# Optimization experiments

Hardware: AMD Instinct MI355X
Metric: run time of the kernel (lower is better)

## Reference

```python
import jax, jax.numpy as jnp
import numpy as np

N = 50000      # nodes
E = 800000     # edges
IN = 128       # in_channels
HID = 32       # hidden_channels per head
HEADS = 4
OUT = 16       # out_channels
NEG_SLOPE_ATT = 0.2   # GATv2Conv default negative_slope
NEG_SLOPE_ACT = 0.01  # F.leaky_relu default
EPS = 1e-16


def setup_inputs() -> dict:
    key = jax.random.key(0)
    ks = jax.random.split(key, 13)
    d1 = HEADS * HID  # 128
    g = lambda k, shape, fan: jax.random.normal(k, shape, jnp.float32) * (1.0 / np.sqrt(fan))
    return {
        "x": jax.random.normal(ks[0], (N, IN), jnp.float32),
        "edge_index": jax.random.randint(ks[1], (2, E), 0, N, dtype=jnp.int32),
        "edge_weight": jax.random.uniform(ks[2], (E,), jnp.float32),
        # conv1 (GATv2): lin_l, lin_r, att, bias
        "Wl1": g(ks[3], (IN, d1), IN), "Wr1": g(ks[4], (IN, d1), IN),
        "att1": g(ks[5], (HEADS, HID), HID), "b1": jnp.zeros((d1,), jnp.float32),
        # conv2
        "Wl2": g(ks[6], (d1, d1), d1), "Wr2": g(ks[7], (d1, d1), d1),
        "att2": g(ks[8], (HEADS, HID), HID), "b2": jnp.zeros((d1,), jnp.float32),
        # classifier
        "Wc": g(ks[9], (d1, OUT), d1), "bc": jnp.zeros((OUT,), jnp.float32),
    }


def gatv2_layer(x, Wl, Wr, att, bias, src, dst):
    n = x.shape[0]
    xl = (x @ Wl).reshape(n, HEADS, HID)  # source transform
    xr = (x @ Wr).reshape(n, HEADS, HID)  # target transform
    m = xl[src] + xr[dst]                                    # [Etot, H, C]
    e = jnp.sum(jax.nn.leaky_relu(m, NEG_SLOPE_ATT) * att, axis=-1)  # [Etot, H]
    # segment softmax over incoming edges of each target node
    emax = jax.ops.segment_max(e, dst, num_segments=n)       # [N, H]
    ex = jnp.exp(e - emax[dst])
    denom = jax.ops.segment_sum(ex, dst, num_segments=n)     # [N, H]
    alpha = ex / (denom[dst] + EPS)                          # [Etot, H]
    out = jax.ops.segment_sum(xl[src] * alpha[:, :, None], dst, num_segments=n)  # [N, H, C]
    return out.reshape(n, HEADS * HID) + bias


def reference(x, edge_index, edge_weight, Wl1, Wr1, att1, b1, Wl2, Wr2, att2, b2, Wc, bc):
    # GATv2Conv default add_self_loops=True
    loops = jnp.arange(N, dtype=edge_index.dtype)
    src = jnp.concatenate([edge_index[0], loops])
    dst = jnp.concatenate([edge_index[1], loops])
    h = gatv2_layer(x, Wl1, Wr1, att1, b1, src, dst)
    h = jax.nn.leaky_relu(h, NEG_SLOPE_ACT)
    h = gatv2_layer(h, Wl2, Wr2, att2, b2, src, dst)
    h = jax.nn.leaky_relu(h, NEG_SLOPE_ACT)
    logits = h @ Wc + bc
    return (logits, h)
```

## Files before the change

kernel.cpp:

```cpp
#include <hip/hip_runtime.h>
#include <hip/hip_fp16.h>


#define LOG2E 1.4426950408889634f
#define AST 40

typedef short bf16x8 __attribute__((ext_vector_type(8)));
typedef float f32x4 __attribute__((ext_vector_type(4)));

__device__ __forceinline__ unsigned short f2bf(float f) {
  union { float f; unsigned u; } x; x.f = f;
  unsigned r = x.u + 0x7fffu + ((x.u >> 16) & 1u);
  return (unsigned short)(r >> 16);
}
__device__ __forceinline__ float bf2f(unsigned short h) {
  union { unsigned u; float f; } x; x.u = ((unsigned)h) << 16;
  return x.f;
}
__device__ __forceinline__ void split4(float4 v, ushort4& h, ushort4& l) {
  h.x = f2bf(v.x); l.x = f2bf(v.x - bf2f(h.x));
  h.y = f2bf(v.y); l.y = f2bf(v.y - bf2f(h.y));
  h.z = f2bf(v.z); l.z = f2bf(v.z - bf2f(h.z));
  h.w = f2bf(v.w); l.w = f2bf(v.w - bf2f(h.w));
}


__global__ __launch_bounds__(256) void zero_i32(int* __restrict__ p, int n) {
  int i = blockIdx.x * 256 + threadIdx.x;
  if (i < n) p[i] = 0;
}

__global__ __launch_bounds__(256) void scan_blk(const int* __restrict__ cnt,
                                                int* __restrict__ excl,
                                                int* __restrict__ bsum, int n) {
  __shared__ int s[256];
  int t = threadIdx.x, i = blockIdx.x * 256 + t;
  int v = (i < n) ? (cnt[i] + 1) : 0;
  s[t] = v;
  __syncthreads();
#pragma unroll
  for (int off = 1; off < 256; off <<= 1) {
    int u = (t >= off) ? s[t - off] : 0;
    __syncthreads();
    s[t] += u;
    __syncthreads();
  }
  if (i < n) excl[i] = s[t] - v;
  if (t == 255) bsum[blockIdx.x] = s[255];
}

__global__ __launch_bounds__(256) void scan_bsum(int* __restrict__ bsum, int nb,
                                                 int* __restrict__ row_start, int n) {
  __shared__ int s[256];
  int t = threadIdx.x;
  int v = (t < nb) ? bsum[t] : 0;
  s[t] = v;
  __syncthreads();
#pragma unroll
  for (int off = 1; off < 256; off <<= 1) {
    int u = (t >= off) ? s[t - off] : 0;
    __syncthreads();
    s[t] += u;
    __syncthreads();
  }
  if (t < nb) bsum[t] = s[t] - v;
  if (t == 255) row_start[n] = s[255];
}

__global__ __launch_bounds__(256) void scan_add(int* __restrict__ row_start,
                                                const int* __restrict__ bsum,
                                                int* __restrict__ wpos,
                                                int* __restrict__ csr,
                                                int n, int padBase) {
  int i = blockIdx.x * 256 + threadIdx.x;
  if (i < n) {
    int r = row_start[i] + bsum[blockIdx.x];
    row_start[i] = r;
    wpos[i] = r + 1;
    csr[r] = i;
  }
  if (blockIdx.x == 0 && threadIdx.x < 16) csr[padBase + threadIdx.x] = 0;
}

__global__ __launch_bounds__(256) void convert_count(
    const float* __restrict__ Wl1, const float* __restrict__ Wr1,
    const float* __restrict__ Wl2, const float* __restrict__ Wr2,
    unsigned short* __restrict__ BT1h, unsigned short* __restrict__ BT1l,
    unsigned short* __restrict__ BT2h, unsigned short* __restrict__ BT2l,
    const int* __restrict__ dst, int* __restrict__ cnt, int E) {
  int b = blockIdx.x;
  if (b >= 256) {
    int i = (b - 256) * 256 + threadIdx.x;
    if (i < E) atomicAdd(&cnt[dst[i]], 1);
    return;
  }
  const float* Wl = (b < 128) ? Wl1 : Wl2;
  const float* Wr = (b < 128) ? Wr1 : Wr2;
  unsigned short* BTh = (b < 128) ? BT1h : BT2h;
  unsigned short* BTl = (b < 128) ? BT1l : BT2l;
  int idx = (b & 127) * 256 + threadIdx.x;
  int col = idx >> 7, k = idx & 127;
  float v = (col < 128) ? Wl[k * 128 + col] : Wr[k * 128 + (col - 128)];
  unsigned short h = f2bf(v);
  BTh[idx] = h;
  BTl[idx] = f2bf(v - bf2f(h));
}

enum { IN_F32 = 0, IN_F16 = 1 };
#define NSCAT 1152
#define NCHUNK 128
template <int MODE, int FUSE>
__global__ __launch_bounds__(256) void gemm_mfma(
    const float* __restrict__ Af, const __half* __restrict__ Af16,
    const unsigned short* __restrict__ BTh, const unsigned short* __restrict__ BTl,
    __half* __restrict__ Cl, __half* __restrict__ Cr, int nrows,
    const int* __restrict__ esrc, const int* __restrict__ edst,
    int* __restrict__ wpos, int* __restrict__ csr, int E, int sliceSize) {
  __shared__ __align__(16) unsigned short smem[4 * 128 * AST];
  int tid = threadIdx.x;
  int bx, by;
  if (FUSE) {
    int g = blockIdx.x / 9, r = blockIdx.x - g * 9;
    if (r < 5) {
      int sid = g * 5 + r;
      if (sid < NSCAT) {
        int slice = blockIdx.x & 7;
        int chunk = (g >> 3) * 5;
        for (int gp = g & ~7; gp < g; ++gp)
          chunk += (((slice - gp) & 7) < 5) ? 1 : 0;
        if (chunk < NCHUNK) {
          int per = (E + NCHUNK - 1) / NCHUNK;
          int b0 = chunk * per;
          int ee = min(b0 + per, E);
          int lo = slice * sliceSize, hi = lo + sliceSize;
          int i = b0 + tid;
          for (; i + 768 < ee; i += 1024) {
            int d0 = edst[i];
            int d1 = edst[i + 256];
            int d2 = edst[i + 512];
            int d3 = edst[i + 768];
            if (d0 >= lo && d0 < hi) {
              int s = esrc[i];
              int p = atomicAdd(&wpos[d0], 1); csr[p] = s;
            }
            if (d1 >= lo && d1 < hi) {
              int s = esrc[i + 256];
              int p = atomicAdd(&wpos[d1], 1); csr[p] = s;
            }
            if (d2 >= lo && d2 < hi) {
              int s = esrc[i + 512];
              int p = atomicAdd(&wpos[d2], 1); csr[p] = s;
            }
            if (d3 >= lo && d3 < hi) {
              int s = esrc[i + 768];
              int p = atomicAdd(&wpos[d3], 1); csr[p] = s;
            }
          }
          for (; i < ee; i += 256) {
            int d = edst[i];
            if (d >= lo && d < hi) {
              int s = esrc[i];
              int p = atomicAdd(&wpos[d], 1); csr[p] = s;
            }
          }
        }
      }
      return;
    }
    int gid = g * 4 + (r - 5);
    int nbx = (nrows + 127) >> 7;
    if (gid >= nbx * 2) return;
    bx = gid >> 1;
    by = gid & 1;
  } else {
    bx = blockIdx.x;
    by = blockIdx.y;
  }

  unsigned short* sAh = smem;
  unsigned short* sAl = smem + 5120;
  unsigned short* sBh = smem + 10240;
  unsigned short* sBl = smem + 15360;

  int wave = tid >> 6, lane = tid & 63;
  int rowBase = bx * 128;
  int colBase = by * 128;
  int rowHalf = (wave >> 1) * 64;
  int colHalf = (wave & 1) * 64;
  int l15 = lane & 15, quad = lane >> 4;

  f32x4 acc[4][4];
#pragma unroll
  for (int m = 0; m < 4; ++m)
#pragma unroll
    for (int n = 0; n < 4; ++n) acc[m][n] = (f32x4){0.f, 0.f, 0.f, 0.f};

  for (int kc = 0; kc < 4; ++kc) {
#pragma unroll
    for (int i = 0; i < 2; ++i) {
      int idx = tid + i * 256;
      int row = idx >> 2, seg = idx & 3;
      int gr = rowBase + row;
      float4 v0 = make_float4(0.f, 0.f, 0.f, 0.f), v1 = v0;
      if (MODE == IN_F32) {
        if (gr < nrows) {
          v0 = *(const float4*)&Af[(size_t)gr * 128 + kc * 32 + seg * 8];
          v1 = *(const float4*)&Af[(size_t)gr * 128 + kc * 32 + seg * 8 + 4];
        }
      } else {
        if (gr < nrows) {
          uint4 raw = *(const uint4*)&Af16[(size_t)gr * 128 + kc * 32 + seg * 8];
          const __half* hp = (const __half*)&raw;
          v0 = make_float4(__half2float(hp[0]), __half2float(hp[1]),
                           __half2float(hp[2]), __half2float(hp[3]));
          v1 = make_float4(__half2float(hp[4]), __half2float(hp[5]),
                           __half2float(hp[6]), __half2float(hp[7]));
        }
      }
      ushort4 h0, l0, h1, l1;
      split4(v0, h0, l0);
      split4(v1, h1, l1);
      *(ushort4*)&sAh[row * AST + seg * 8] = h0;
      *(ushort4*)&sAh[row * AST + seg * 8 + 4] = h1;
      *(ushort4*)&sAl[row * AST + seg * 8] = l0;
      *(ushort4*)&sAl[row * AST + seg * 8 + 4] = l1;
    }
#pragma unroll
    for (int i = 0; i < 2; ++i) {
      int idx = tid + i * 256;
      int col = idx >> 2, seg = idx & 3;
      *(uint4*)&sBh[col * AST + seg * 8] =
          *(const uint4*)&BTh[(size_t)(colBase + col) * 128 + kc * 32 + seg * 8];
      *(uint4*)&sBl[col * AST + seg * 8] =
          *(const uint4*)&BTl[(size_t)(colBase + col) * 128 + kc * 32 + seg * 8];
    }
    __syncthreads();

    bf16x8 afh[4], afl[4], bfh[4], bfl[4];
#pragma unroll
    for (int m = 0; m < 4; ++m) {
      int r = rowHalf + m * 16 + l15;
      afh[m] = *(const bf16x8*)&sAh[r * AST + quad * 8];
      afl[m] = *(const bf16x8*)&sAl[r * AST + quad * 8];
    }
#pragma unroll
    for (int n = 0; n < 4; ++n) {
      int cc = colHalf + n * 16 + l15;
      bfh[n] = *(const bf16x8*)&sBh[cc * AST + quad * 8];
      bfl[n] = *(const bf16x8*)&sBl[cc * AST + quad * 8];
    }
    __builtin_amdgcn_s_setprio(1);
#pragma unroll
    for (int m = 0; m < 4; ++m)
#pragma unroll
      for (int n = 0; n < 4; ++n) {
        acc[m][n] = __builtin_amdgcn_mfma_f32_16x16x32_bf16(afh[m], bfh[n], acc[m][n], 0, 0, 0);
        acc[m][n] = __builtin_amdgcn_mfma_f32_16x16x32_bf16(afh[m], bfl[n], acc[m][n], 0, 0, 0);
        acc[m][n] = __builtin_amdgcn_mfma_f32_16x16x32_bf16(afl[m], bfh[n], acc[m][n], 0, 0, 0);
      }
    __builtin_amdgcn_s_setprio(0);
    __syncthreads();
  }

  __half* __restrict__ C = (by == 0) ? Cl : Cr;
#pragma unroll
  for (int m = 0; m < 4; ++m)
#pragma unroll
    for (int r = 0; r < 4; ++r) {
      int grow = rowBase + rowHalf + m * 16 + quad * 4 + r;
      if (grow < nrows) {
#pragma unroll
        for (int n = 0; n < 4; ++n)
          C[(size_t)grow * 128 + colHalf + n * 16 + l15] = __float2half(acc[m][n][r]);
      }
    }
}

__global__ __launch_bounds__(256) void gat_attn(const __half* __restrict__ xl,
                                                const __half* __restrict__ xr,
                                                const int* __restrict__ row_start,
                                                const int* __restrict__ csr,
                                                const float* __restrict__ att,
                                                const float* __restrict__ bias,
                                                float* __restrict__ ofp,
                                                __half* __restrict__ oh16,
                                                int n_nodes) {
  int node = blockIdx.x * 4 + (threadIdx.x >> 6);
  if (node >= n_nodes) return;
  int lane = threadIdx.x & 63;
  int slot = lane >> 4;
  int l15 = lane & 15;
  int c0 = l15 * 8;

  float fxr[8];
  {
    uint4 raw = *(const uint4*)&xr[(size_t)node * 128 + c0];
    const __half* hp = (const __half*)&raw;
#pragma unroll
    for (int k = 0; k < 8; ++k) fxr[k] = __half2float(hp[k]);
  }
  float a06[8], a04[8];
  {
    float4 a0 = *(const float4*)&att[c0];
    float4 a1 = *(const float4*)&att[c0 + 4];
    float av[8] = {a0.x, a0.y, a0.z, a0.w, a1.x, a1.y, a1.z, a1.w};
    const float C06 = 0.6f * LOG2E, C04 = 0.4f * LOG2E;
#pragma unroll
    for (int k = 0; k < 8; ++k) { a06[k] = av[k] * C06; a04[k] = av[k] * C04; }
  }

  float acc[8];
#pragma unroll
  for (int k = 0; k < 8; ++k) acc[k] = 0.f;
  float lsum = 0.f;

#define EDGE_BODY(SRC, PVALID)                                                 \
  {                                                                            \
    uint4 raw = *(const uint4*)&xl[(size_t)(unsigned)(SRC)*128 + c0];          \
    const __half* hp = (const __half*)&raw;                                    \
    float e = 0.f;                                                             \
    _Pragma("unroll") for (int k = 0; k < 8; ++k) {                            \
      float t = __half2float(hp[k]) + fxr[k];                                  \
      e = fmaf(a06[k], t, e);                                                  \
      e = fmaf(a04[k], fabsf(t), e);                                           \
    }                                                                          \
    e += __shfl_xor(e, 1);                                                     \
    e += __shfl_xor(e, 2);                                                     \
    float p = (PVALID) ? __builtin_amdgcn_exp2f(e) : 0.f;                      \
    lsum += p;                                                                 \
    _Pragma("unroll") for (int k = 0; k < 8; ++k)                              \
        acc[k] = fmaf(p, __half2float(hp[k]), acc[k]);                         \
  }

  int beg = row_start[node], end = row_start[node + 1];
  int deg = end - beg;
  int fullEnd = beg + (deg & ~15);

  for (int base = beg; base < fullEnd; base += 16) {
    int b0 = base + 4 * slot;
    int s0 = csr[b0], s1 = csr[b0 + 1], s2 = csr[b0 + 2], s3 = csr[b0 + 3];
    EDGE_BODY(s0, true);
    EDGE_BODY(s1, true);
    EDGE_BODY(s2, true);
    EDGE_BODY(s3, true);
  }
  for (int base = fullEnd; base < end; base += 4) {
    int idx = base + slot;
    int src = csr[idx];
    EDGE_BODY(src, idx < end);
  }
#undef EDGE_BODY

  lsum += __shfl_xor(lsum, 16);
  lsum += __shfl_xor(lsum, 32);
#pragma unroll
  for (int k = 0; k < 8; ++k) {
    acc[k] += __shfl_xor(acc[k], 16);
    acc[k] += __shfl_xor(acc[k], 32);
  }

  if (slot == 0) {
    float4 b0v = *(const float4*)&bias[c0];
    float4 b1v = *(const float4*)&bias[c0 + 4];
    float bv[8] = {b0v.x, b0v.y, b0v.z, b0v.w, b1v.x, b1v.y, b1v.z, b1v.w};
    float inv = 1.f / (lsum + 1e-16f);
    float o[8];
#pragma unroll
    for (int k = 0; k < 8; ++k) {
      float v = fmaf(acc[k], inv, bv[k]);
      o[k] = fmaf(0.495f, fabsf(v), 0.505f * v);
    }
    if (ofp) {
      *(float4*)&ofp[(size_t)node * 128 + c0] = make_float4(o[0], o[1], o[2], o[3]);
      *(float4*)&ofp[(size_t)node * 128 + c0 + 4] = make_float4(o[4], o[5], o[6], o[7]);
    }
    if (oh16) {
      ushort4 ha, hb;
      ha.x = __half_as_ushort(__float2half(o[0]));
      ha.y = __half_as_ushort(__float2half(o[1]));
      ha.z = __half_as_ushort(__float2half(o[2]));
      ha.w = __half_as_ushort(__float2half(o[3]));
      hb.x = __half_as_ushort(__float2half(o[4]));
      hb.y = __half_as_ushort(__float2half(o[5]));
      hb.z = __half_as_ushort(__float2half(o[6]));
      hb.w = __half_as_ushort(__float2half(o[7]));
      *(ushort4*)&oh16[(size_t)node * 128 + c0] = ha;
      *(ushort4*)&oh16[(size_t)node * 128 + c0 + 4] = hb;
    }
  }
}

__global__ __launch_bounds__(256) void classifier_kernel(const float4* __restrict__ h4,
                                                         const float* __restrict__ Wc,
                                                         const float* __restrict__ bc,
                                                         float* __restrict__ logits,
                                                         int n) {
  __shared__ float sW[2048];
  __shared__ float sb[16];
  int t = threadIdx.x;
#pragma unroll
  for (int i = 0; i < 8; ++i) sW[t + i * 256] = Wc[t + i * 256];
  if (t < 16) sb[t] = bc[t];
  __syncthreads();
  int node = blockIdx.x * 256 + t;
  if (node >= n) return;
  float acc[16];
#pragma unroll
  for (int o = 0; o < 16; ++o) acc[o] = sb[o];
  for (int c4 = 0; c4 < 32; ++c4) {
    float4 hv = h4[(unsigned)node * 32 + c4];
    const float* w = &sW[c4 * 64];
#pragma unroll
    for (int o = 0; o < 16; ++o) {
      acc[o] = fmaf(hv.x, w[o], acc[o]);
      acc[o] = fmaf(hv.y, w[16 + o], acc[o]);
      acc[o] = fmaf(hv.z, w[32 + o], acc[o]);
      acc[o] = fmaf(hv.w, w[48 + o], acc[o]);
    }
  }
#pragma unroll
  for (int q = 0; q < 4; ++q)
    *(float4*)&logits[(size_t)node * 16 + q * 4] =
        make_float4(acc[q * 4], acc[q * 4 + 1], acc[q * 4 + 2], acc[q * 4 + 3]);
}


extern "C" void kernel_launch(void* const* d_in, const int* in_sizes, int n_in,
                              void* d_out, int out_size, void* d_ws, size_t ws_size,
                              hipStream_t stream) {
  const float* x    = (const float*)d_in[0];
  const int*   ei   = (const int*)d_in[1];
  const float* Wl1  = (const float*)d_in[3];
  const float* Wr1  = (const float*)d_in[4];
  const float* att1 = (const float*)d_in[5];
  const float* b1   = (const float*)d_in[6];
  const float* Wl2  = (const float*)d_in[7];
  const float* Wr2  = (const float*)d_in[8];
  const float* att2 = (const float*)d_in[9];
  const float* b2   = (const float*)d_in[10];
  const float* Wc   = (const float*)d_in[11];
  const float* bc   = (const float*)d_in[12];

  const int N = in_sizes[0] / 128;
  const int E = in_sizes[1] / 2;

  float* outp   = (float*)d_out;
  float* logits = outp;
  float* hout   = outp + (size_t)N * 16;
  __half* h1f16 = (__half*)hout;

  char* ws = (char*)d_ws;
  __half* xlbuf = (__half*)ws;                ws += (size_t)N * 128 * 2;
  __half* xrbuf = (__half*)ws;                ws += (size_t)N * 128 * 2;
  unsigned short* WT1h = (unsigned short*)ws; ws += 256 * 128 * 2;
  unsigned short* WT1l = (unsigned short*)ws; ws += 256 * 128 * 2;
  unsigned short* WT2h = (unsigned short*)ws; ws += 256 * 128 * 2;
  unsigned short* WT2l = (unsigned short*)ws; ws += 256 * 128 * 2;
  int* cnt       = (int*)ws;                  ws += (size_t)N * 4;
  int* row_start = (int*)ws;                  ws += (size_t)(N + 1) * 4;
  int* wpos      = (int*)ws;                  ws += (size_t)N * 4;
  int* bsum      = (int*)ws;                  ws += 256 * 4;
  int* csr       = (int*)ws;                  ws += (size_t)(E + N + 16) * 4;

  const int* esrc = ei;
  const int* edst = ei + E;

  int gN = (N + 255) / 256, gE = (E + 255) / 256;
  int gAttn = (N + 3) / 4;
  int sliceSize = (N + 7) / 8;

  int nbx = (N + 127) / 128;
  int nGemm = nbx * 2;
  int groups = (NSCAT + 4) / 5;
  int g2 = (nGemm + 3) / 4;
  if (g2 > groups) groups = g2;
  int gFused = groups * 9;

  zero_i32<<<gN, 256, 0, stream>>>(cnt, N);
  convert_count<<<256 + gE, 256, 0, stream>>>(Wl1, Wr1, Wl2, Wr2,
                                              WT1h, WT1l, WT2h, WT2l,
                                              edst, cnt, E);
  scan_blk<<<gN, 256, 0, stream>>>(cnt, row_start, bsum, N);
  scan_bsum<<<1, 256, 0, stream>>>(bsum, gN, row_start, N);
  scan_add<<<gN, 256, 0, stream>>>(row_start, bsum, wpos, csr, N, E + N);

  gemm_mfma<IN_F32, 1><<<gFused, 256, 0, stream>>>(
      x, nullptr, WT1h, WT1l, xlbuf, xrbuf, N,
      esrc, edst, wpos, csr, E, sliceSize);
  gat_attn<<<gAttn, 256, 0, stream>>>(xlbuf, xrbuf, row_start, csr, att1, b1,
                                      nullptr, h1f16, N);

  gemm_mfma<IN_F16, 0><<<dim3(nbx, 2), 256, 0, stream>>>(
      nullptr, h1f16, WT2h, WT2l, xlbuf, xrbuf, N,
      nullptr, nullptr, nullptr, nullptr, 0, 0);
  gat_attn<<<gAttn, 256, 0, stream>>>(xlbuf, xrbuf, row_start, csr, att2, b2,
                                      hout, nullptr, N);

  classifier_kernel<<<(N + 255) / 256, 256, 0, stream>>>((const float4*)hout, Wc, bc,
                                                         logits, N);
}
```

Baseline: 314.3 us.

## Pre-bucket edges by destination slice during counting to avoid rescanning all edges

The counting kernel now also partitions edges into 8 destination-slice buckets of (src,dst) pairs, using shared-memory ranks and one global atomic per block per slice. The fused GEMM's scatter blocks then read only their slice's bucket instead of scanning every edge and filtering by range. This removes the roughly 8x redundant reads of the edge list in the scatter phase, at the cost of an extra bucket write pass and a fixed per-slice capacity that could overflow on skewed destination distributions. The separate zeroing kernel is replaced by a memset that also clears the bucket cursors.

```diff
diff --git a/kernel.cpp b/kernel.cpp
--- a/kernel.cpp
+++ b/kernel.cpp
@@ -24,11 +24,6 @@
   h.w = f2bf(v.w); l.w = f2bf(v.w - bf2f(h.w));
 }
 
-
-__global__ __launch_bounds__(256) void zero_i32(int* __restrict__ p, int n) {
-  int i = blockIdx.x * 256 + threadIdx.x;
-  if (i < n) p[i] = 0;
-}
 
 __global__ __launch_bounds__(256) void scan_blk(const int* __restrict__ cnt,
                                                 int* __restrict__ excl,
@@ -82,23 +77,54 @@
   if (blockIdx.x == 0 && threadIdx.x < 16) csr[padBase + threadIdx.x] = 0;
 }
 
+#define EPB 1024
 __global__ __launch_bounds__(256) void convert_count(
     const float* __restrict__ Wl1, const float* __restrict__ Wr1,
     const float* __restrict__ Wl2, const float* __restrict__ Wr2,
     unsigned short* __restrict__ BT1h, unsigned short* __restrict__ BT1l,
     unsigned short* __restrict__ BT2h, unsigned short* __restrict__ BT2l,
-    const int* __restrict__ dst, int* __restrict__ cnt, int E) {
+    const int* __restrict__ esrc, const int* __restrict__ edst,
+    int* __restrict__ cnt, int* __restrict__ bucketCur,
+    int2* __restrict__ bucket, int E, int sliceSize, int cap) {
   int b = blockIdx.x;
+  int t = threadIdx.x;
   if (b >= 256) {
-    int i = (b - 256) * 256 + threadIdx.x;
-    if (i < E) atomicAdd(&cnt[dst[i]], 1);
+    __shared__ int bcnt[8], bbase[8];
+    if (t < 8) bcnt[t] = 0;
+    __syncthreads();
+    int base = (b - 256) * EPB;
+    int sl[4], rk[4], dv[4], sv[4];
+#pragma unroll
+    for (int j = 0; j < 4; ++j) {
+      int i = base + t + j * 256;
+      bool v = (i < E);
+      int d = v ? edst[i] : 0;
+      sv[j] = v ? esrc[i] : 0;
+      dv[j] = d;
+      int s = d / sliceSize;
+      sl[j] = v ? s : -1;
+      if (v) {
+        atomicAdd(&cnt[d], 1);
+        rk[j] = atomicAdd(&bcnt[s], 1);
+      }
+    }
+    __syncthreads();
+    if (t < 8 && bcnt[t] > 0) bbase[t] = atomicAdd(&bucketCur[t], bcnt[t]);
+    __syncthreads();
+#pragma unroll
+    for (int j = 0; j < 4; ++j) {
+      if (sl[j] >= 0) {
+        int pos = sl[j] * cap + bbase[sl[j]] + rk[j];
+        bucket[pos] = make_int2(sv[j], dv[j]);
+      }
+    }
     return;
   }
   const float* Wl = (b < 128) ? Wl1 : Wl2;
   const float* Wr = (b < 128) ? Wr1 : Wr2;
   unsigned short* BTh = (b < 128) ? BT1h : BT2h;
   unsigned short* BTl = (b < 128) ? BT1l : BT2l;
-  int idx = (b & 127) * 256 + threadIdx.x;
+  int idx = (b & 127) * 256 + t;
   int col = idx >> 7, k = idx & 127;
   float v = (col < 128) ? Wl[k * 128 + col] : Wr[k * 128 + (col - 128)];
   unsigned short h = f2bf(v);
@@ -114,8 +140,8 @@
     const float* __restrict__ Af, const __half* __restrict__ Af16,
     const unsigned short* __restrict__ BTh, const unsigned short* __restrict__ BTl,
     __half* __restrict__ Cl, __half* __restrict__ Cr, int nrows,
-    const int* __restrict__ esrc, const int* __restrict__ edst,
-    int* __restrict__ wpos, int* __restrict__ csr, int E, int sliceSize) {
+    const int2* __restrict__ bucket, const int* __restrict__ bucketCur,
+    int* __restrict__ wpos, int* __restrict__ csr, int cap) {
   __shared__ __align__(16) unsigned short smem[4 * 128 * AST];
   int tid = threadIdx.x;
   int bx, by;
@@ -129,39 +155,21 @@
         for (int gp = g & ~7; gp < g; ++gp)
           chunk += (((slice - gp) & 7) < 5) ? 1 : 0;
         if (chunk < NCHUNK) {
-          int per = (E + NCHUNK - 1) / NCHUNK;
+          int cntS = bucketCur[slice];
+          int per = (cntS + NCHUNK - 1) / NCHUNK;
           int b0 = chunk * per;
-          int ee = min(b0 + per, E);
-          int lo = slice * sliceSize, hi = lo + sliceSize;
+          int ee = min(b0 + per, cntS);
+          const int2* bk = bucket + (size_t)slice * cap;
           int i = b0 + tid;
-          for (; i + 768 < ee; i += 1024) {
-            int d0 = edst[i];
-            int d1 = edst[i + 256];
-            int d2 = edst[i + 512];
-            int d3 = edst[i + 768];
-            if (d0 >= lo && d0 < hi) {
-              int s = esrc[i];
-              int p = atomicAdd(&wpos[d0], 1); csr[p] = s;
-            }
-            if (d1 >= lo && d1 < hi) {
-              int s = esrc[i + 256];
-              int p = atomicAdd(&wpos[d1], 1); csr[p] = s;
-            }
-            if (d2 >= lo && d2 < hi) {
-              int s = esrc[i + 512];
-              int p = atomicAdd(&wpos[d2], 1); csr[p] = s;
-            }
-            if (d3 >= lo && d3 < hi) {
-              int s = esrc[i + 768];
-              int p = atomicAdd(&wpos[d3], 1); csr[p] = s;
-            }
+          for (; i + 256 < ee; i += 512) {
+            int2 e0 = bk[i];
+            int2 e1 = bk[i + 256];
+            int p0 = atomicAdd(&wpos[e0.y], 1); csr[p0] = e0.x;
+            int p1 = atomicAdd(&wpos[e1.y], 1); csr[p1] = e1.x;
           }
           for (; i < ee; i += 256) {
-            int d = edst[i];
-            if (d >= lo && d < hi) {
-              int s = esrc[i];
-              int p = atomicAdd(&wpos[d], 1); csr[p] = s;
-            }
+            int2 e = bk[i];
+            int p = atomicAdd(&wpos[e.y], 1); csr[p] = e.x;
           }
         }
       }
@@ -449,6 +457,8 @@
   float* hout   = outp + (size_t)N * 16;
   __half* h1f16 = (__half*)hout;
 
+  const int cap = E / 8 + 16384;
+
   char* ws = (char*)d_ws;
   __half* xlbuf = (__half*)ws;                ws += (size_t)N * 128 * 2;
   __half* xrbuf = (__half*)ws;                ws += (size_t)N * 128 * 2;
@@ -457,15 +467,17 @@
   unsigned short* WT2h = (unsigned short*)ws; ws += 256 * 128 * 2;
   unsigned short* WT2l = (unsigned short*)ws; ws += 256 * 128 * 2;
   int* cnt       = (int*)ws;                  ws += (size_t)N * 4;
-  int* row_start = (int*)ws;                  ws += (size_t)(N + 1) * 4;
+  int* bucketCur = (int*)ws;                  ws += 8 * 4;
   int* wpos      = (int*)ws;                  ws += (size_t)N * 4;
   int* bsum      = (int*)ws;                  ws += 256 * 4;
+  int2* bucket   = (int2*)ws;                 ws += (size_t)8 * cap * 8;
+  int* row_start = (int*)ws;                  ws += (size_t)(N + 1) * 4;
   int* csr       = (int*)ws;                  ws += (size_t)(E + N + 16) * 4;
 
   const int* esrc = ei;
   const int* edst = ei + E;
 
-  int gN = (N + 255) / 256, gE = (E + 255) / 256;
+  int gN = (N + 255) / 256;
   int gAttn = (N + 3) / 4;
   int sliceSize = (N + 7) / 8;
 
@@ -476,23 +488,23 @@
   if (g2 > groups) groups = g2;
   int gFused = groups * 9;
 
-  zero_i32<<<gN, 256, 0, stream>>>(cnt, N);
-  convert_count<<<256 + gE, 256, 0, stream>>>(Wl1, Wr1, Wl2, Wr2,
-                                              WT1h, WT1l, WT2h, WT2l,
-                                              edst, cnt, E);
+  hipMemsetAsync(cnt, 0, (size_t)(N + 8) * 4, stream);
+  convert_count<<<256 + (E + EPB - 1) / EPB, 256, 0, stream>>>(
+      Wl1, Wr1, Wl2, Wr2, WT1h, WT1l, WT2h, WT2l,
+      esrc, edst, cnt, bucketCur, bucket, E, sliceSize, cap);
   scan_blk<<<gN, 256, 0, stream>>>(cnt, row_start, bsum, N);
   scan_bsum<<<1, 256, 0, stream>>>(bsum, gN, row_start, N);
   scan_add<<<gN, 256, 0, stream>>>(row_start, bsum, wpos, csr, N, E + N);
 
   gemm_mfma<IN_F32, 1><<<gFused, 256, 0, stream>>>(
       x, nullptr, WT1h, WT1l, xlbuf, xrbuf, N,
-      esrc, edst, wpos, csr, E, sliceSize);
+      bucket, bucketCur, wpos, csr, cap);
   gat_attn<<<gAttn, 256, 0, stream>>>(xlbuf, xrbuf, row_start, csr, att1, b1,
                                       nullptr, h1f16, N);
 
   gemm_mfma<IN_F16, 0><<<dim3(nbx, 2), 256, 0, stream>>>(
       nullptr, h1f16, WT2h, WT2l, xlbuf, xrbuf, N,
-      nullptr, nullptr, nullptr, nullptr, 0, 0);
+      nullptr, nullptr, nullptr, nullptr, 0);
   gat_attn<<<gAttn, 256, 0, stream>>>(xlbuf, xrbuf, row_start, csr, att2, b2,
                                       hout, nullptr, N);
 
```

After: 307.0 us. 2.3% less time.
